# Kernel optimization log

Hardware: AMD Instinct MI355X
Metric: run time of the kernel (lower is better)

The kernel has to match this reference:

```python
import jax, jax.numpy as jnp
import numpy as np

SIGMA = 25.0
N, E, F, D = 10000, 160000, 256, 3


def setup_inputs() -> dict:
    key = jax.random.key(0)
    ks = jax.random.split(key, 24)
    s = 0.02
    inp = {
        "x": jax.random.normal(ks[0], (N, D), jnp.float32),
        "edge_index": jax.random.randint(ks[1], (2, E), 0, N, jnp.int64),
        "t": jax.random.uniform(ks[2], (N, 1), jnp.float32, 1e-3, 1.0),
        "emb_pcs": jax.random.normal(ks[3], (N, F), jnp.float32),
        # x_encoder
        "enc_W": jax.random.normal(ks[4], (D, F), jnp.float32) * s,
        "enc_b": jnp.zeros((F,), jnp.float32),
        # GaussianFourierProjection (scale=30, fixed) + Linear
        "fourier_W": jax.random.normal(ks[5], (F // 2,), jnp.float32) * 30.0,
        "te_W": jax.random.normal(ks[6], (F, F), jnp.float32) * s,
        "te_b": jnp.zeros((F,), jnp.float32),
        # mlp1 / mlp2: Linear(6F,F) -> ReLU -> Linear(F,F)
        "m1_W1": jax.random.normal(ks[7], (6 * F, F), jnp.float32) * s,
        "m1_b1": jnp.zeros((F,), jnp.float32),
        "m1_W2": jax.random.normal(ks[8], (F, F), jnp.float32) * s,
        "m1_b2": jnp.zeros((F,), jnp.float32),
        "m2_W1": jax.random.normal(ks[9], (6 * F, F), jnp.float32) * s,
        "m2_b1": jnp.zeros((F,), jnp.float32),
        "m2_W2": jax.random.normal(ks[10], (F, F), jnp.float32) * s,
        "m2_b2": jnp.zeros((F,), jnp.float32),
        # mlp3: Linear(6F,F) -> ReLU -> Linear(F,D)
        "m3_W1": jax.random.normal(ks[11], (6 * F, F), jnp.float32) * s,
        "m3_b1": jnp.zeros((F,), jnp.float32),
        "m3_W2": jax.random.normal(ks[12], (F, D), jnp.float32) * s,
        "m3_b2": jnp.zeros((D,), jnp.float32),
    }
    return inp


def _edge_conv(h, src, dst, W1, b1, W2, b2, n):
    # PyG EdgeConv: out_i = max_{j->i} MLP([x_i, x_j - x_i])
    hi = h[dst]                                             # [E, 3F]
    e = jnp.concatenate([hi, h[src] - hi], axis=-1)         # [E, 6F]
    e = jax.nn.relu(e @ W1 + b1) @ W2 + b2                  # [E, out]
    out = jax.ops.segment_max(e, dst, num_segments=n)
    return jnp.where(jnp.isfinite(out), out, 0.0)           # empty segments -> 0


def reference(x, edge_index, t, emb_pcs,
              enc_W, enc_b, fourier_W, te_W, te_b,
              m1_W1, m1_b1, m1_W2, m1_b2,
              m2_W1, m2_b1, m2_W2, m2_b2,
              m3_W1, m3_b1, m3_W2, m3_b2):
    src, dst = edge_index[0], edge_index[1]
    n = x.shape[0]
    # time embedding: Fourier projection -> Linear -> swish
    tv = t[:, 0]
    proj = tv[:, None] * fourier_W[None, :] * (2.0 * np.pi)  # [N, F/2]
    temb = jnp.concatenate([jnp.sin(proj), jnp.cos(proj)], axis=-1) @ te_W + te_b
    temb = temb * jax.nn.sigmoid(temb)                       # [N, F]
    h = x @ enc_W + enc_b                                    # [N, F]
    h = jnp.concatenate([h, temb, emb_pcs], axis=-1)         # [N, 3F]
    h = jax.nn.relu(_edge_conv(h, src, dst, m1_W1, m1_b1, m1_W2, m1_b2, n))
    h = jnp.concatenate([h, temb, emb_pcs], axis=-1)
    h = jax.nn.relu(_edge_conv(h, src, dst, m2_W1, m2_b1, m2_W2, m2_b2, n))
    h = jnp.concatenate([h, temb, emb_pcs], axis=-1)
    h = _edge_conv(h, src, dst, m3_W1, m3_b1, m3_W2, m3_b2, n)  # [N, D]
    # marginal_prob_std(t) = sqrt((sigma^(2t) - 1) / (2 ln sigma))
    std = jnp.sqrt((jnp.power(SIGMA, 2.0 * t) - 1.0) / (2.0 * jnp.log(SIGMA)))
    return h / (std + 1e-7)
```

## Files before the change

kernel.cpp:

```cpp
#include <hip/hip_runtime.h>
#include <hip/hip_bf16.h>
#include <math.h>

#define HC 768
#define DPB 8

typedef __attribute__((ext_vector_type(8))) short bf16x8;
typedef __attribute__((ext_vector_type(4))) float f32x4;

__device__ __forceinline__ float bf2f(unsigned short h) {
    return __uint_as_float(((unsigned)h) << 16);
}
__device__ __forceinline__ unsigned short f2bf(float f) {
    unsigned u = __float_as_uint(f);
    return (unsigned short)((u + 0x7fffu + ((u >> 16) & 1u)) >> 16);
}
__device__ __forceinline__ unsigned pack_bf2(float a, float b) {
    __hip_bfloat162 h = __float22bfloat162_rn(make_float2(a, b));
    return *reinterpret_cast<unsigned*>(&h);
}

__device__ __forceinline__ unsigned enc_f(float f) {
    unsigned u = __float_as_uint(f);
    return (u & 0x80000000u) ? ~u : (u | 0x80000000u);
}
__device__ __forceinline__ float dec_f(unsigned e) {
    unsigned u = (e & 0x80000000u) ? (e & 0x7FFFFFFFu) : ~e;
    return __uint_as_float(u);
}
#define ENC_NEG_INF 0x007FFFFFu

__global__ void pre_and_prep_kernel(const float* __restrict__ x,
                                    const float* __restrict__ t,
                                    const float* __restrict__ emb,
                                    const float* __restrict__ enc_W,
                                    const float* __restrict__ enc_b,
                                    const float* __restrict__ fw,
                                    const float* __restrict__ te_W,
                                    const float* __restrict__ te_b,
                                    unsigned short* __restrict__ hcat,
                                    float* __restrict__ invstd,
                                    const float* __restrict__ W1a,
                                    const float* __restrict__ W1b,
                                    const float* __restrict__ W1c,
                                    const float* __restrict__ W2a,
                                    const float* __restrict__ W2b,
                                    const float* __restrict__ W2c,
                                    unsigned short* __restrict__ WcatT,
                                    unsigned short* __restrict__ W2T,
                                    unsigned short* __restrict__ W2T3,
                                    int N, int nPre) {
    __shared__ float smem[64 * 65];
    const int tid = threadIdx.x;

    if ((int)blockIdx.x < nPre) {
        float (*ti)[256] = (float(*)[256])smem;
        float* tv = smem + 8 * 256;
        const int n0 = blockIdx.x * 8;

        if (tid < 8) {
            int n = n0 + tid;
            float tt = (n < N) ? t[n] : 1.0f;
            tv[tid] = tt;
            const float ln_s = 3.2188758248682006f;
            float p = expf(2.0f * tt * ln_s);
            float sd = sqrtf((p - 1.0f) / (2.0f * ln_s));
            if (n < N) invstd[n] = 1.0f / (sd + 1e-7f);
        }
        __syncthreads();

        const float TWO_PI = 6.283185307179586f;
        for (int p = tid; p < 8 * 128; p += 256) {
            int n = p >> 7, j = p & 127;
            float pr = tv[n] * fw[j] * TWO_PI;
            ti[n][j]       = sinf(pr);
            ti[n][j + 128] = cosf(pr);
        }
        __syncthreads();

        const int j = tid;
        float acc[8];
#pragma unroll
        for (int n = 0; n < 8; ++n) acc[n] = 0.f;
        for (int k = 0; k < 256; ++k) {
            float w = te_W[k * 256 + j];
#pragma unroll
            for (int n = 0; n < 8; ++n) acc[n] += ti[n][k] * w;
        }
        float bj  = te_b[j];
        float ew0 = enc_W[0 * 256 + j], ew1 = enc_W[1 * 256 + j], ew2 = enc_W[2 * 256 + j];
        float ebj = enc_b[j];
        for (int n = 0; n < 8; ++n) {
            int node = n0 + n;
            if (node >= N) break;
            float v = acc[n] + bj;
            float temb = v / (1.0f + expf(-v));
            float h0 = x[node * 3 + 0] * ew0 + x[node * 3 + 1] * ew1 +
                       x[node * 3 + 2] * ew2 + ebj;
            hcat[(size_t)node * HC + j]       = f2bf(h0);
            hcat[(size_t)node * HC + 256 + j] = f2bf(temb);
            hcat[(size_t)node * HC + 512 + j] = f2bf(emb[node * 256 + j]);
        }
    } else {
        float (*buf)[65] = (float(*)[65])smem;
        const int bid = blockIdx.x - nPre;
        const int tx = tid & 63, ty = tid >> 6;

        if (bid < 288) {
            const int l = bid / 96, r = bid - l * 96;
            const float* W1 = (l == 0) ? W1a : (l == 1) ? W1b : W1c;
            unsigned short* WT = WcatT + (size_t)l * 512 * 768;
            const int k0 = (r % 12) * 64, n0 = (r / 12) * 64;
#pragma unroll
            for (int i = 0; i < 16; ++i) {
                int kl = ty + i * 4;
                int k = k0 + kl, n = n0 + tx;
                float v = (n < 256) ? (W1[(size_t)k * 256 + n] - W1[(size_t)(k + 768) * 256 + n])
                                    : W1[(size_t)(k + 768) * 256 + (n - 256)];
                buf[kl][tx] = v;
            }
            __syncthreads();
#pragma unroll
            for (int i = 0; i < 16; ++i) {
                int nl = ty + i * 4;
                WT[(size_t)(n0 + nl) * 768 + k0 + tx] = f2bf(buf[tx][nl]);
            }
        } else if (bid < 320) {
            const int m = bid - 288, l = m >> 4, r = m & 15;
            const float* W2 = (l == 0) ? W2a : W2b;
            unsigned short* WT = W2T + (size_t)l * 256 * 256;
            const int k0 = (r & 3) * 64, n0 = (r >> 2) * 64;
#pragma unroll
            for (int i = 0; i < 16; ++i) {
                int kl = ty + i * 4;
                buf[kl][tx] = W2[(size_t)(k0 + kl) * 256 + n0 + tx];
            }
            __syncthreads();
#pragma unroll
            for (int i = 0; i < 16; ++i) {
                int nl = ty + i * 4;
                WT[(size_t)(n0 + nl) * 256 + k0 + tx] = f2bf(buf[tx][nl]);
            }
        } else {
            int idx = (bid - 320) * 256 + tid;
            int n = idx >> 8, k = idx & 255;
            W2T3[idx] = (n < 3) ? f2bf(W2c[(size_t)k * 3 + n]) : (unsigned short)0;
        }
    }
}

__global__ __launch_bounds__(256)
void node_gemm_mfma_kernel(const unsigned short* __restrict__ A,
                           const unsigned short* __restrict__ BT,
                           const float* __restrict__ b1,
                           unsigned short* __restrict__ C,
                           int M) {
    const int row0 = blockIdx.x * 64, col0 = blockIdx.y * 128;
    const int tid = threadIdx.x;
    const int wv = tid >> 6, lane = tid & 63;
    const int q = lane >> 4, nl = lane & 15;
    const int rbase = row0 + (wv >> 1) * 32;
    const int cbase = col0 + (wv & 1) * 64;

    int r0c = min(rbase + nl, M - 1);
    int r1c = min(rbase + 16 + nl, M - 1);
    const unsigned short* pa0 = A + (size_t)r0c * HC + q * 8;
    const unsigned short* pa1 = A + (size_t)r1c * HC + q * 8;

    f32x4 acc[2][4];
#pragma unroll
    for (int s = 0; s < 2; ++s)
#pragma unroll
        for (int t = 0; t < 4; ++t) acc[s][t] = (f32x4){0.f, 0.f, 0.f, 0.f};

    for (int ks = 0; ks < 24; ++ks) {
        const int k0 = ks * 32;
        const bf16x8 av0 = *(const bf16x8*)(pa0 + k0);
        const bf16x8 av1 = *(const bf16x8*)(pa1 + k0);
#pragma unroll
        for (int t = 0; t < 4; ++t) {
            const bf16x8 bv = *(const bf16x8*)(BT + (size_t)(cbase + t * 16 + nl) * 768 + k0 + q * 8);
            acc[0][t] = __builtin_amdgcn_mfma_f32_16x16x32_bf16(av0, bv, acc[0][t], 0, 0, 0);
            acc[1][t] = __builtin_amdgcn_mfma_f32_16x16x32_bf16(av1, bv, acc[1][t], 0, 0, 0);
        }
    }

#pragma unroll
    for (int s = 0; s < 2; ++s) {
        const int rr = rbase + s * 16 + q * 4;
#pragma unroll
        for (int t = 0; t < 4; ++t) {
            int col = cbase + t * 16 + nl;
            float bb = (col < 256) ? b1[col] : 0.f;
#pragma unroll
            for (int i = 0; i < 4; ++i) {
                int r = rr + i;
                if (r < M) C[(size_t)r * 512 + col] = f2bf(acc[s][t][i] + bb);
            }
        }
    }
}

__global__ void init_kernel(unsigned* __restrict__ cnt, unsigned* __restrict__ seg3, int N) {
    int idx = blockIdx.x * 256 + threadIdx.x;
    if (idx < 2 * N) cnt[idx] = 0u;
    else if (idx < 5 * N) seg3[idx - 2 * N] = ENC_NEG_INF;
}
__global__ void hist_kernel(const int* __restrict__ dst, unsigned* __restrict__ cnt, int E) {
    int e = blockIdx.x * 256 + threadIdx.x;
    if (e < E) atomicAdd(&cnt[dst[e]], 1u);
}
__global__ void scan_kernel(const unsigned* __restrict__ cnt,
                            int* __restrict__ row_start, int N) {
    __shared__ unsigned wexc[16];
    __shared__ unsigned chunk_total;
    __shared__ unsigned carry;
    const int tid = threadIdx.x, wv = tid >> 6, ln = tid & 63;
    if (tid == 0) carry = 0u;
    __syncthreads();
    for (int base = 0; base < N; base += 1024) {
        int i = base + tid;
        unsigned v = (i < N) ? cnt[i] : 0u;
        unsigned s = v;
#pragma unroll
        for (int off = 1; off < 64; off <<= 1) {
            unsigned o = __shfl_up(s, off);
            if (ln >= off) s += o;
        }
        if (ln == 63) wexc[wv] = s;
        __syncthreads();
        if (tid < 16) {
            unsigned ws = wexc[tid];
            unsigned tt = ws;
#pragma unroll
            for (int off = 1; off < 16; off <<= 1) {
                unsigned o = __shfl_up(tt, off);
                if (tid >= off) tt += o;
            }
            wexc[tid] = tt - ws;
            if (tid == 15) chunk_total = tt;
        }
        __syncthreads();
        if (i < N) row_start[i] = (int)(carry + wexc[wv] + s - v);
        __syncthreads();
        if (tid == 0) carry += chunk_total;
        __syncthreads();
    }
    if (tid == 0) row_start[N] = (int)carry;
}
__global__ void scatter_kernel(const int* __restrict__ src, const int* __restrict__ dst,
                               const int* __restrict__ row_start,
                               unsigned* __restrict__ wcnt,
                               int* __restrict__ es, int* __restrict__ ed, int E) {
    int e = blockIdx.x * 256 + threadIdx.x;
    if (e >= E) return;
    int d = dst[e];
    int pos = row_start[d] + (int)atomicAdd(&wcnt[d], 1u);
    es[pos] = src[e];
    ed[pos] = d;
}

__global__ __launch_bounds__(256, 3)
void edge_seg_gemm_kernel(const unsigned short* __restrict__ RQb,
                          const int* __restrict__ es,
                          const int* __restrict__ ed,
                          const int* __restrict__ row_start,
                          const unsigned short* __restrict__ W2T,
                          const float* __restrict__ b2,
                          unsigned short* __restrict__ hcat,
                          int N, int E) {
    __shared__ unsigned short af[32][264];
    __shared__ unsigned short rdst[DPB][256];
    __shared__ unsigned lseg[DPB * 256];
    __shared__ int ss[32], sdl[32];
    const int d0 = blockIdx.x * DPB;
    const int tid = threadIdx.x;
    const int wv = tid >> 6, lane = tid & 63;
    const int q = lane >> 4, nl = lane & 15;

    for (int i = tid; i < DPB * 256; i += 256) lseg[i] = ENC_NEG_INF;

    {
        int rrow = tid >> 5;
        int kc = (tid & 31) * 8;
        int d = d0 + rrow;
        int dc = (d < N) ? d : (N - 1);
        *(bf16x8*)&rdst[rrow][kc] = *(const bf16x8*)(RQb + (size_t)dc * 512 + kc);
    }

    const int eBeg = row_start[d0];
    const int eEnd = row_start[min(d0 + DPB, N)];

    for (int c0 = eBeg; c0 < eEnd; c0 += 32) {
        __syncthreads();
        if (tid < 32) {
            int e = c0 + tid;
            ss[tid]  = (e < eEnd) ? es[e] : 0;
            sdl[tid] = (e < eEnd) ? (ed[e] - d0) : -1;
        }
        __syncthreads();

        {
            const int el = tid >> 3;
            const int kc = (tid & 7) * 32;
            int dl = sdl[el];
            int dla = (dl >= 0) ? dl : 0;
            int srow = ss[el];
            const unsigned short* ps = RQb + (size_t)srow * 512 + 256 + kc;
#pragma unroll
            for (int j = 0; j < 4; ++j) {
                bf16x8 dv = *(const bf16x8*)&rdst[dla][kc + j * 8];
                bf16x8 sv = *(const bf16x8*)(ps + j * 8);
                float f[8];
#pragma unroll
                for (int u = 0; u < 8; ++u)
                    f[u] = fmaxf(bf2f((unsigned short)dv[u]) + bf2f((unsigned short)sv[u]), 0.f);
                uint4 o;
                o.x = pack_bf2(f[0], f[1]);
                o.y = pack_bf2(f[2], f[3]);
                o.z = pack_bf2(f[4], f[5]);
                o.w = pack_bf2(f[6], f[7]);
                *(uint4*)&af[el][kc + j * 8] = o;
            }
        }
        __syncthreads();

#pragma unroll
        for (int sub = 0; sub < 2; ++sub) {
            f32x4 acc[4];
#pragma unroll
            for (int t = 0; t < 4; ++t) acc[t] = (f32x4){0.f, 0.f, 0.f, 0.f};
#pragma unroll
            for (int ks = 0; ks < 8; ++ks) {
                const bf16x8 av = *(const bf16x8*)&af[sub * 16 + nl][ks * 32 + q * 8];
#pragma unroll
                for (int t = 0; t < 4; ++t) {
                    const bf16x8 bv = *(const bf16x8*)(W2T +
                        (size_t)(wv * 64 + t * 16 + nl) * 256 + ks * 32 + q * 8);
                    acc[t] = __builtin_amdgcn_mfma_f32_16x16x32_bf16(av, bv, acc[t], 0, 0, 0);
                }
            }
            const int m0 = sub * 16 + q * 4;
            int dls[4];
#pragma unroll
            for (int i = 0; i < 4; ++i) dls[i] = sdl[m0 + i];
#pragma unroll
            for (int t = 0; t < 4; ++t) {
                const int col = wv * 64 + t * 16 + nl;
                float cur = -INFINITY;
                int cd = dls[0];
#pragma unroll
                for (int i = 0; i < 4; ++i) {
                    int dl = dls[i];
                    if (dl != cd) {
                        if (cd >= 0) atomicMax(&lseg[cd * 256 + col], enc_f(cur));
                        cur = -INFINITY; cd = dl;
                    }
                    cur = fmaxf(cur, acc[t][i]);
                }
                if (cd >= 0) atomicMax(&lseg[cd * 256 + col], enc_f(cur));
            }
        }
    }
    __syncthreads();

    for (int i = tid; i < DPB * 256; i += 256) {
        int dl = i >> 8, col = i & 255;
        int d = d0 + dl;
        if (d >= N) continue;
        float f = dec_f(lseg[i]);
        float v = isfinite(f) ? fmaxf(f + b2[col], 0.f) : 0.f;
        hcat[(size_t)d * HC + col] = f2bf(v);
    }
}

__global__ __launch_bounds__(256)
void edge3_mfma_kernel(const unsigned short* __restrict__ RQb,
                       const int* __restrict__ es,
                       const int* __restrict__ ed,
                       const unsigned short* __restrict__ W2T3,
                       const float* __restrict__ b2,
                       unsigned* __restrict__ seg3,
                       int E) {
    const int wave = blockIdx.x * 4 + (threadIdx.x >> 6);
    const int lane = threadIdx.x & 63;
    const int q = lane >> 4, nl = lane & 15;
    const int e0 = wave * 16;
    if (e0 >= E) return;

    bf16x8 bv[8];
#pragma unroll
    for (int ks = 0; ks < 8; ++ks)
        bv[ks] = *(const bf16x8*)(W2T3 + (size_t)nl * 256 + ks * 32 + q * 8);

    int eA = e0 + nl;
    int eAc = (eA < E) ? eA : (E - 1);
    const int dA = ed[eAc], sA = es[eAc];
    const unsigned short* pd = RQb + (size_t)dA * 512 + q * 8;
    const unsigned short* ps = RQb + (size_t)sA * 512 + 256 + q * 8;

    f32x4 acc = (f32x4){0.f, 0.f, 0.f, 0.f};
#pragma unroll
    for (int ks = 0; ks < 8; ++ks) {
        bf16x8 dv = *(const bf16x8*)(pd + ks * 32);
        bf16x8 sv = *(const bf16x8*)(ps + ks * 32);
        float f[8];
#pragma unroll
        for (int u = 0; u < 8; ++u)
            f[u] = fmaxf(bf2f((unsigned short)dv[u]) + bf2f((unsigned short)sv[u]), 0.f);
        uint4 o;
        o.x = pack_bf2(f[0], f[1]);
        o.y = pack_bf2(f[2], f[3]);
        o.z = pack_bf2(f[4], f[5]);
        o.w = pack_bf2(f[6], f[7]);
        bf16x8 av = *(bf16x8*)&o;
        acc = __builtin_amdgcn_mfma_f32_16x16x32_bf16(av, bv[ks], acc, 0, 0, 0);
    }

    if (nl < 3) {
        float bb = b2[nl];
        float cur = -INFINITY;
        int cd = -2;
#pragma unroll
        for (int i = 0; i < 4; ++i) {
            int e = e0 + q * 4 + i;
            int d = (e < E) ? ed[e] : -1;
            if (d != cd) {
                if (cd >= 0) atomicMax(&seg3[(size_t)cd * 3 + nl], enc_f(cur + bb));
                cur = -INFINITY; cd = d;
            }
            if (d >= 0) cur = fmaxf(cur, acc[i]);
        }
        if (cd >= 0) atomicMax(&seg3[(size_t)cd * 3 + nl], enc_f(cur + bb));
    }
}

__global__ void finalize3_kernel(const unsigned* __restrict__ seg3,
                                 const float* __restrict__ invstd,
                                 float* __restrict__ out, int N) {
    int idx = blockIdx.x * 256 + threadIdx.x;
    if (idx >= N * 3) return;
    int n = idx / 3;
    float f = dec_f(seg3[idx]);
    if (!isfinite(f)) f = 0.f;
    out[idx] = f * invstd[n];
}

extern "C" void kernel_launch(void* const* d_in, const int* in_sizes, int n_in,
                              void* d_out, int out_size, void* d_ws, size_t ws_size,
                              hipStream_t stream) {
    const float* x     = (const float*)d_in[0];
    const int*   ei    = (const int*)d_in[1];
    const float* t     = (const float*)d_in[2];
    const float* emb   = (const float*)d_in[3];
    const float* enc_W = (const float*)d_in[4];
    const float* enc_b = (const float*)d_in[5];
    const float* fw    = (const float*)d_in[6];
    const float* te_W  = (const float*)d_in[7];
    const float* te_b  = (const float*)d_in[8];
    const float* W1[3] = {(const float*)d_in[9],  (const float*)d_in[13], (const float*)d_in[17]};
    const float* b1[3] = {(const float*)d_in[10], (const float*)d_in[14], (const float*)d_in[18]};
    const float* W2[3] = {(const float*)d_in[11], (const float*)d_in[15], (const float*)d_in[19]};
    const float* b2[3] = {(const float*)d_in[12], (const float*)d_in[16], (const float*)d_in[20]};

    const int N = in_sizes[2];
    const int E = in_sizes[1] / 2;
    const int* src = ei;
    const int* dst = ei + E;

    char* ws = (char*)d_ws;
    unsigned short* hcat  = (unsigned short*)ws; ws += (size_t)N * HC * 2;
    unsigned short* RQb   = (unsigned short*)ws; ws += (size_t)N * 512 * 2;
    unsigned short* WcatT = (unsigned short*)ws; ws += (size_t)3 * 512 * 768 * 2;
    unsigned short* W2T   = (unsigned short*)ws; ws += (size_t)2 * 256 * 256 * 2;
    unsigned short* W2T3  = (unsigned short*)ws; ws += (size_t)16 * 256 * 2;
    unsigned* seg3        = (unsigned*)ws;       ws += (size_t)N * 3 * 4;
    float*    invstd      = (float*)ws;          ws += (size_t)N * 4;
    int*      es          = (int*)ws;            ws += (size_t)E * 4;
    int*      ed          = (int*)ws;            ws += (size_t)E * 4;
    unsigned* cnt         = (unsigned*)ws;       ws += (size_t)N * 4;
    unsigned* wcnt        = (unsigned*)ws;       ws += (size_t)N * 4;
    int*      row_start   = (int*)ws;            ws += (size_t)(N + 1) * 4;

    init_kernel<<<(5 * N + 255) / 256, 256, 0, stream>>>(cnt, seg3, N);
    hist_kernel<<<(E + 255) / 256, 256, 0, stream>>>(dst, cnt, E);
    scan_kernel<<<1, 1024, 0, stream>>>(cnt, row_start, N);
    scatter_kernel<<<(E + 255) / 256, 256, 0, stream>>>(src, dst, row_start, wcnt, es, ed, E);

    const int nPre = (N + 7) / 8;
    pre_and_prep_kernel<<<nPre + 336, 256, 0, stream>>>(
        x, t, emb, enc_W, enc_b, fw, te_W, te_b, hcat, invstd,
        W1[0], W1[1], W1[2], W2[0], W2[1], W2[2], WcatT, W2T, W2T3, N, nPre);

    for (int l = 0; l < 3; ++l) {
        dim3 gn((N + 63) / 64, 4);
        node_gemm_mfma_kernel<<<gn, 256, 0, stream>>>(
            hcat, WcatT + (size_t)l * 512 * 768, b1[l], RQb, N);
        if (l < 2) {
            edge_seg_gemm_kernel<<<(N + DPB - 1) / DPB, 256, 0, stream>>>(
                RQb, es, ed, row_start, W2T + (size_t)l * 256 * 256, b2[l], hcat, N, E);
        } else {
            int chunks = (E + 15) / 16;
            edge3_mfma_kernel<<<(chunks + 3) / 4, 256, 0, stream>>>(
                RQb, es, ed, W2T3, b2[l], seg3, E);
            finalize3_kernel<<<(N * 3 + 255) / 256, 256, 0, stream>>>(seg3, invstd, (float*)d_out, N);
        }
    }
}
```

Baseline: 485.5 us.

## Fuse CSR build kernels into one cooperative grid-synced kernel

Replaces the four separate init/histogram/scan/scatter launches with a single cooperative kernel of 64 blocks that uses grid.sync between phases and a two-level block scan. The goal is to cut launch overhead and the serial single-block scan. In exchange, only 64 blocks do the histogram and scatter atomics, which limits parallelism, and grid syncs add their own cost. The old four-kernel path is kept as a fallback if the cooperative launch fails.

```diff
diff --git a/kernel.cpp b/kernel.cpp
--- a/kernel.cpp
+++ b/kernel.cpp
@@ -1,6 +1,9 @@
 #include <hip/hip_runtime.h>
 #include <hip/hip_bf16.h>
+#include <hip/hip_cooperative_groups.h>
 #include <math.h>
+
+namespace cg = cooperative_groups;
 
 #define HC 768
 #define DPB 8
@@ -201,6 +204,77 @@
     }
 }
 
+#define SORTB 64
+__global__ void sort_coop_kernel(const int* __restrict__ src,
+                                 const int* __restrict__ dst,
+                                 unsigned* __restrict__ cnt,
+                                 int* __restrict__ row_start,
+                                 unsigned* __restrict__ seg3,
+                                 int* __restrict__ es, int* __restrict__ ed,
+                                 unsigned* __restrict__ blk_sums,
+                                 int N, int E) {
+    cg::grid_group grid = cg::this_grid();
+    __shared__ unsigned wsum[4];
+    const int tid = threadIdx.x;
+    const int gid = blockIdx.x * 256 + tid;
+    const int gsz = SORTB * 256;
+    const int wv = tid >> 6, ln = tid & 63;
+
+    for (int i = gid; i < 2 * N; i += gsz) cnt[i] = 0u;
+    for (int i = gid; i < 3 * N; i += gsz) seg3[i] = ENC_NEG_INF;
+    grid.sync();
+
+    for (int e = gid; e < E; e += gsz) atomicAdd(&cnt[dst[e]], 1u);
+    grid.sync();
+
+    const int SEG = (N + SORTB - 1) / SORTB;
+    const int base = blockIdx.x * SEG;
+    const int i = base + tid;
+    unsigned v = (tid < SEG && i < N) ? cnt[i] : 0u;
+    unsigned s = v;
+#pragma unroll
+    for (int off = 1; off < 64; off <<= 1) {
+        unsigned o = __shfl_up(s, off);
+        if (ln >= off) s += o;
+    }
+    if (ln == 63) wsum[wv] = s;
+    __syncthreads();
+    unsigned woff = 0;
+#pragma unroll
+    for (int w = 0; w < 4; ++w) { if (w < wv) woff += wsum[w]; }
+    unsigned incl = s + woff;
+    if (tid < SEG && i < N) row_start[i] = (int)(incl - v);
+    if (tid == 255) blk_sums[blockIdx.x] = incl;
+    grid.sync();
+
+    if (blockIdx.x == 0 && tid < SORTB) {
+        unsigned bv = blk_sums[tid];
+        unsigned bs = bv;
+#pragma unroll
+        for (int off = 1; off < 64; off <<= 1) {
+            unsigned o = __shfl_up(bs, off);
+            if (tid >= off) bs += o;
+        }
+        blk_sums[tid] = bs - bv;
+    }
+    grid.sync();
+
+    {
+        unsigned boff = blk_sums[blockIdx.x];
+        if (tid < SEG && i < N) row_start[i] += (int)boff;
+        if (gid == 0) row_start[N] = E;
+    }
+    grid.sync();
+
+    unsigned* wcnt = cnt + N;
+    for (int e = gid; e < E; e += gsz) {
+        int d = dst[e];
+        int pos = row_start[d] + (int)atomicAdd(&wcnt[d], 1u);
+        es[pos] = src[e];
+        ed[pos] = d;
+    }
+}
+
 __global__ void init_kernel(unsigned* __restrict__ cnt, unsigned* __restrict__ seg3, int N) {
     int idx = blockIdx.x * 256 + threadIdx.x;
     if (idx < 2 * N) cnt[idx] = 0u;
@@ -481,11 +555,25 @@
     unsigned* cnt         = (unsigned*)ws;       ws += (size_t)N * 4;
     unsigned* wcnt        = (unsigned*)ws;       ws += (size_t)N * 4;
     int*      row_start   = (int*)ws;            ws += (size_t)(N + 1) * 4;
-
-    init_kernel<<<(5 * N + 255) / 256, 256, 0, stream>>>(cnt, seg3, N);
-    hist_kernel<<<(E + 255) / 256, 256, 0, stream>>>(dst, cnt, E);
-    scan_kernel<<<1, 1024, 0, stream>>>(cnt, row_start, N);
-    scatter_kernel<<<(E + 255) / 256, 256, 0, stream>>>(src, dst, row_start, wcnt, es, ed, E);
+    unsigned* blk_sums    = (unsigned*)ws;       ws += (size_t)SORTB * 4;
+
+    {
+        const int* src_a = src; const int* dst_a = dst;
+        unsigned* cnt_a = cnt; int* rs_a = row_start; unsigned* seg3_a = seg3;
+        int* es_a = es; int* ed_a = ed; unsigned* bs_a = blk_sums;
+        int N_a = N, E_a = E;
+        void* args[] = {(void*)&src_a, (void*)&dst_a, (void*)&cnt_a, (void*)&rs_a,
+                        (void*)&seg3_a, (void*)&es_a, (void*)&ed_a, (void*)&bs_a,
+                        (void*)&N_a, (void*)&E_a};
+        hipError_t err = hipLaunchCooperativeKernel((void*)sort_coop_kernel,
+                                                    dim3(SORTB), dim3(256), args, 0, stream);
+        if (err != hipSuccess) {
+            init_kernel<<<(5 * N + 255) / 256, 256, 0, stream>>>(cnt, seg3, N);
+            hist_kernel<<<(E + 255) / 256, 256, 0, stream>>>(dst, cnt, E);
+            scan_kernel<<<1, 1024, 0, stream>>>(cnt, row_start, N);
+            scatter_kernel<<<(E + 255) / 256, 256, 0, stream>>>(src, dst, row_start, wcnt, es, ed, E);
+        }
+    }
 
     const int nPre = (N + 7) / 8;
     pre_and_prep_kernel<<<nPre + 336, 256, 0, stream>>>(
```

Result: slower. 560.7 us (+15.5%).
